# Kernel tuning notes

Measured on AMD Instinct MI355X. Metric: run time of the kernel, lower is better.

Reference implementation:

```python
import jax, jax.numpy as jnp
import numpy as np

E = 2048   # embed_dim
H = 16     # num query heads
D = E // H # head_dim = 128
B = 2
S = 2048


def setup_inputs() -> dict:
    key = jax.random.key(0)
    ks = jax.random.split(key, 12)
    sc = 0.02
    return {
        "input": jax.random.normal(ks[0], (B, S, E), jnp.float32),
        "kv": jax.random.normal(ks[1], (B, S, E), jnp.float32),
        "Wq": jax.random.normal(ks[2], (E, E), jnp.float32) * sc,
        "bq": jnp.zeros((E,), jnp.float32),
        "Wk": jax.random.normal(ks[3], (D, E), jnp.float32) * sc,
        "bk": jnp.zeros((D,), jnp.float32),
        "Wv": jax.random.normal(ks[4], (D, E), jnp.float32) * sc,
        "bv": jnp.zeros((D,), jnp.float32),
        "Wo": jax.random.normal(ks[5], (E, E), jnp.float32) * sc,
        "bo": jnp.zeros((E,), jnp.float32),
        "expanding_context": 0,
    }


def reference(input, kv, Wq, bq, Wk, bk, Wv, bv, Wo, bo, expanding_context):
    b, s, _ = input.shape
    # projections (torch Linear: x @ W.T + b)
    q = (input @ Wq.T + bq).reshape(b, s, H, D).transpose(0, 2, 1, 3)  # [B,H,S,D]
    k = kv @ Wk.T + bk  # [B,S,D] single KV head
    v = kv @ Wv.T + bv  # [B,S,D]
    # scores with single KV head broadcast across query heads
    scores = jnp.einsum('bhsd,btd->bhst', q, k) / jnp.sqrt(jnp.float32(D))
    causal = jnp.triu(jnp.ones((s, s), bool), k=1)  # True above diagonal
    scores = jnp.where(causal[None, None], jnp.float32(-jnp.inf), scores)
    attn = jax.nn.softmax(scores, axis=-1)
    out = jnp.einsum('bhst,btd->bhsd', attn, v)  # [B,H,S,D]
    out = out.transpose(0, 2, 1, 3).reshape(b, s, E)
    return out @ Wo.T + bo
```

## Files before the change

### kernel.cpp

```cpp
#include <hip/hip_runtime.h>

#define B_  2
#define S_  2048
#define E_  2048
#define H_  16
#define D_  128
#define BS_ (B_*S_)

typedef __bf16 bf16_t;
typedef __bf16 bf16x8 __attribute__((ext_vector_type(8)));
typedef __bf16 bf16x4 __attribute__((ext_vector_type(4)));
typedef float  f32x4  __attribute__((ext_vector_type(4)));
typedef float  f32x16 __attribute__((ext_vector_type(16)));

#define QSCALE 0.1275174131003543f

__device__ __forceinline__ void gld16(const bf16_t* g, bf16_t* l) {
    __builtin_amdgcn_global_load_lds(
        (const __attribute__((address_space(1))) void*)g,
        (__attribute__((address_space(3))) void*)l,
        16, 0, 0);
}

__global__ void cvt_all(const float* __restrict__ s0, const float* __restrict__ s1,
                        const float* __restrict__ s2, const float* __restrict__ s3,
                        const float* __restrict__ s4, const float* __restrict__ s5,
                        bf16_t* d0, bf16_t* d1, bf16_t* d2,
                        bf16_t* d3, bf16_t* d4, bf16_t* d5)
{
    long i = ((long)blockIdx.x * blockDim.x + threadIdx.x) * 4;
    const float* s; bf16_t* d;
    if      (i <  8388608) { s = s0; d = d0; }
    else if (i < 16777216) { s = s1; d = d1; i -=  8388608; }
    else if (i < 20971520) { s = s2; d = d2; i -= 16777216; }
    else if (i < 21233664) { s = s3; d = d3; i -= 20971520; }
    else if (i < 21495808) { s = s4; d = d4; i -= 21233664; }
    else                   { s = s5; d = d5; i -= 21495808; }
    float4 v = *(const float4*)(s + i);
    bf16x4 o;
    o[0] = (bf16_t)v.x; o[1] = (bf16_t)v.y; o[2] = (bf16_t)v.z; o[3] = (bf16_t)v.w;
    *(bf16x4*)(d + i) = o;
}

template<int EP>
__device__ __forceinline__ void gemm_tile64(
    const bf16_t* __restrict__ A, const bf16_t* __restrict__ W,
    const float* __restrict__ biasA, const float* __restrict__ biasB,
    float* __restrict__ Cf, bf16_t* __restrict__ Cb,
    int N, int K, float scale, int m0, int w_n0, int c_n0,
    bf16_t* As, bf16_t* Bs)
{
    const int tid  = threadIdx.x;
    const int wave = tid >> 6, lane = tid & 63;
    const int wm = wave >> 1, wn = wave & 1;
    const int lrow = lane & 15, quad = lane >> 4;
    const int r8 = lane >> 3, c8 = (lane & 7) << 3;

    f32x4 acc[4][2] = {};

    for (int k0 = 0; k0 < K; k0 += 64) {
        __syncthreads();
#pragma unroll
        for (int j = 0; j < 4; ++j) {
            int base = (wave * 4 + j) * 8;
            gld16(A + (size_t)(m0 + base + r8) * K + k0 + c8, &As[base * 64]);
        }
#pragma unroll
        for (int j = 0; j < 2; ++j) {
            int base = (wave * 2 + j) * 8;
            gld16(W + (size_t)(w_n0 + base + r8) * K + k0 + c8, &Bs[base * 64]);
        }
        __syncthreads();
#pragma unroll
        for (int ks = 0; ks < 2; ++ks) {
            bf16x8 af[4], bfr[2];
#pragma unroll
            for (int mt = 0; mt < 4; ++mt)
                af[mt] = *(const bf16x8*)&As[(wm * 64 + mt * 16 + lrow) * 64 + ks * 32 + quad * 8];
#pragma unroll
            for (int nt = 0; nt < 2; ++nt)
                bfr[nt] = *(const bf16x8*)&Bs[(wn * 32 + nt * 16 + lrow) * 64 + ks * 32 + quad * 8];
#pragma unroll
            for (int mt = 0; mt < 4; ++mt)
#pragma unroll
                for (int nt = 0; nt < 2; ++nt)
                    acc[mt][nt] = __builtin_amdgcn_mfma_f32_16x16x32_bf16(
                        af[mt], bfr[nt], acc[mt][nt], 0, 0, 0);
        }
    }

#pragma unroll
    for (int mt = 0; mt < 4; ++mt) {
#pragma unroll
        for (int nt = 0; nt < 2; ++nt) {
            int nn = wn * 32 + nt * 16 + lrow;
            int col = c_n0 + nn;
            float bvv = (EP == 1 && biasB && col >= 128) ? biasB[col - 128]
                                                         : biasA[col];
#pragma unroll
            for (int r = 0; r < 4; ++r) {
                int row = m0 + wm * 64 + mt * 16 + quad * 4 + r;
                float v = (acc[mt][nt][r] + bvv) * scale;
                if (EP == 0) Cf[(size_t)row * N + col] = v;
                else         Cb[(size_t)row * N + col] = (bf16_t)v;
            }
        }
    }
}

__global__ __launch_bounds__(256) void gemm_qkv(
    const bf16_t* __restrict__ xb, const bf16_t* __restrict__ kvb,
    const bf16_t* __restrict__ Wq, const bf16_t* __restrict__ Wkv,
    const float* __restrict__ bq, const float* __restrict__ bk,
    const float* __restrict__ bv,
    bf16_t* __restrict__ Qb, bf16_t* __restrict__ KVb)
{
    __shared__ __align__(16) bf16_t As[128 * 64];
    __shared__ __align__(16) bf16_t Bs[64 * 64];
    const int m0 = blockIdx.y * 128;
    if (blockIdx.x < 32) {
        int n0 = blockIdx.x * 64;
        gemm_tile64<1>(xb, Wq, bq, nullptr, nullptr, Qb, E_, E_, QSCALE,
                       m0, n0, n0, As, Bs);
    } else {
        int n0 = (blockIdx.x - 32) * 64;
        gemm_tile64<1>(kvb, Wkv, bk, bv, nullptr, KVb, 256, E_, 1.0f,
                       m0, n0, n0, As, Bs);
    }
}

__global__ __launch_bounds__(256) void gemm_o(
    const bf16_t* __restrict__ A, const bf16_t* __restrict__ W,
    const float* __restrict__ bias, float* __restrict__ Cf)
{
    __shared__ __align__(16) bf16_t As[128 * 64];
    __shared__ __align__(16) bf16_t Bs[64 * 64];
    int n0 = blockIdx.x * 64;
    gemm_tile64<0>(A, W, bias, nullptr, Cf, nullptr, E_, E_, 1.0f,
                   blockIdx.y * 128, n0, n0, As, Bs);
}

__global__ __launch_bounds__(256, 2) void mqa_attn(
    const bf16_t* __restrict__ Q, const bf16_t* __restrict__ KV,
    bf16_t* __restrict__ O)
{
    __shared__ __align__(16) bf16_t Kt[64][136];
    __shared__ __align__(16) bf16_t Vt[128][72];
    __shared__ float rsl[4][32];

    const int bx = blockIdx.x, h = blockIdx.y, b = blockIdx.z;
    const int qb = b ? bx : (15 - bx);
    const int tid = threadIdx.x, wave = tid >> 6, lane = tid & 63;
    const int ln = lane & 31, hi = lane >> 5;
    const int q0w = qb * 128 + wave * 32;

    const bf16_t* kvp = KV + (size_t)(b * S_) * 256;

    bf16x8 qf[8];
    {
        const bf16_t* qp = Q + ((size_t)(b * S_ + q0w + ln)) * E_ + h * D_ + hi * 8;
#pragma unroll
        for (int st = 0; st < 8; ++st) qf[st] = *(const bf16x8*)(qp + st * 16);
    }

    f32x16 oacc[4] = {};
    float rs = 0.f;

    const int ntiles = 2 * qb + 2;
    bf16x8 kreg[4], vreg[4];

#pragma unroll
    for (int i = 0; i < 4; ++i) {
        int c = tid + 256 * i;
        kreg[i] = *(const bf16x8*)(kvp + (size_t)(c >> 4) * 256 + ((c & 15) << 3));
        vreg[i] = *(const bf16x8*)(kvp + (size_t)(c & 63) * 256 + 128 + ((c >> 6) << 3));
    }

    for (int kt = 0; kt < ntiles; ++kt) {
        const int k_base = kt * 64;
        __syncthreads();
#pragma unroll
        for (int i = 0; i < 4; ++i) {
            int c = tid + 256 * i;
            *(bf16x8*)&Kt[c >> 4][(c & 15) << 3] = kreg[i];
            int n = c & 63, d0 = (c >> 6) << 3;
#pragma unroll
            for (int j = 0; j < 8; ++j) Vt[d0 + j][n] = vreg[i][j];
        }
        __syncthreads();
        if (kt + 1 < ntiles) {
            const int nb = (kt + 1) * 64;
#pragma unroll
            for (int i = 0; i < 4; ++i) {
                int c = tid + 256 * i;
                kreg[i] = *(const bf16x8*)(kvp + (size_t)(nb + (c >> 4)) * 256 + ((c & 15) << 3));
                vreg[i] = *(const bf16x8*)(kvp + (size_t)(nb + (c & 63)) * 256 + 128 + ((c >> 6) << 3));
            }
        }

        if (k_base <= q0w + 31) {
            f32x16 sc[2] = {f32x16{}, f32x16{}};
#pragma unroll
            for (int st = 0; st < 8; ++st) {
                bf16x8 qv = qf[st];
#pragma unroll
                for (int ct = 0; ct < 2; ++ct) {
                    bf16x8 kf = *(const bf16x8*)&Kt[ct * 32 + ln][st * 16 + hi * 8];
                    sc[ct] = __builtin_amdgcn_mfma_f32_32x32x16_bf16(kf, qv, sc[ct], 0, 0, 0);
                }
            }
            const int qi = q0w + ln;
            const bool diag = (k_base + 63 > q0w);
#pragma unroll
            for (int ct = 0; ct < 2; ++ct) {
#pragma unroll
                for (int r = 0; r < 16; ++r) {
                    float s = sc[ct][r];
                    if (diag) {
                        int kj = k_base + ct * 32 + (r & 3) + 8 * (r >> 2) + 4 * hi;
                        if (kj > qi) s = -1e30f;
                    }
                    float p = exp2f(fminf(s, 110.f));
                    rs += p;
                    sc[ct][r] = p;
                }
            }
            bf16x8 af[4];
#pragma unroll
            for (int ks = 0; ks < 4; ++ks) {
                const int c = ks >> 1, b8 = (ks & 1) * 8;
                union { bf16_t h[2]; unsigned u; } pk0, pk1, pk2, pk3;
                pk0.h[0] = (bf16_t)sc[c][b8 + 0]; pk0.h[1] = (bf16_t)sc[c][b8 + 1];
                pk1.h[0] = (bf16_t)sc[c][b8 + 2]; pk1.h[1] = (bf16_t)sc[c][b8 + 3];
                pk2.h[0] = (bf16_t)sc[c][b8 + 4]; pk2.h[1] = (bf16_t)sc[c][b8 + 5];
                pk3.h[0] = (bf16_t)sc[c][b8 + 6]; pk3.h[1] = (bf16_t)sc[c][b8 + 7];
                const unsigned U0 = pk0.u, U1 = pk1.u, U2 = pk2.u, U3 = pk3.u;
                const unsigned V0 = __shfl_xor(U0, 32);
                const unsigned V1 = __shfl_xor(U1, 32);
                const unsigned V2 = __shfl_xor(U2, 32);
                const unsigned V3 = __shfl_xor(U3, 32);
                union { unsigned u[4]; bf16x8 v; } W;
                W.u[0] = hi ? V2 : U0;
                W.u[1] = hi ? V3 : U1;
                W.u[2] = hi ? U2 : V0;
                W.u[3] = hi ? U3 : V1;
                af[ks] = W.v;
            }
#pragma unroll
            for (int ks = 0; ks < 4; ++ks)
#pragma unroll
                for (int t = 0; t < 4; ++t) {
                    bf16x8 vf = *(const bf16x8*)&Vt[t * 32 + ln][ks * 16 + hi * 8];
                    oacc[t] = __builtin_amdgcn_mfma_f32_32x32x16_bf16(af[ks], vf, oacc[t], 0, 0, 0);
                }
        }
    }

    rs += __shfl_xor(rs, 32);
    __syncthreads();
    if (lane < 32) rsl[wave][ln] = 1.0f / rs;
    __syncthreads();
#pragma unroll
    for (int t = 0; t < 4; ++t)
#pragma unroll
        for (int r = 0; r < 16; ++r) {
            int ro = (r & 3) + 8 * (r >> 2) + 4 * hi;
            O[((size_t)(b * S_ + q0w + ro)) * E_ + h * D_ + t * 32 + ln] =
                (bf16_t)(oacc[t][r] * rsl[wave][ro]);
        }
}

extern "C" void kernel_launch(void* const* d_in, const int* in_sizes, int n_in,
                              void* d_out, int out_size, void* d_ws, size_t ws_size,
                              hipStream_t stream)
{
    const float* x   = (const float*)d_in[0];
    const float* kv  = (const float*)d_in[1];
    const float* Wq  = (const float*)d_in[2];
    const float* bq  = (const float*)d_in[3];
    const float* Wk  = (const float*)d_in[4];
    const float* bk  = (const float*)d_in[5];
    const float* Wv  = (const float*)d_in[6];
    const float* bv  = (const float*)d_in[7];
    const float* Wo  = (const float*)d_in[8];
    const float* bo  = (const float*)d_in[9];
    float* out = (float*)d_out;

    bf16_t* p    = (bf16_t*)d_ws;
    bf16_t* xb   = p;  p += (size_t)BS_ * E_;
    bf16_t* kvb  = p;  p += (size_t)BS_ * E_;
    bf16_t* Wqb  = p;  p += (size_t)E_ * E_;
    bf16_t* Wkvb = p;  p += (size_t)2 * D_ * E_;
    bf16_t* Wob  = p;  p += (size_t)E_ * E_;
    bf16_t* Qb   = p;  p += (size_t)BS_ * E_;
    bf16_t* KVb  = p;  p += (size_t)BS_ * 256;
    bf16_t* Ob   = p;  p += (size_t)BS_ * E_;

    cvt_all<<<dim3(25088), dim3(256), 0, stream>>>(
        x, kv, Wq, Wk, Wv, Wo,
        xb, kvb, Wqb, Wkvb, Wkvb + (size_t)D_ * E_, Wob);

    gemm_qkv<<<dim3(36, BS_ / 128), 256, 0, stream>>>(
        xb, kvb, Wqb, Wkvb, bq, bk, bv, Qb, KVb);

    mqa_attn<<<dim3(S_ / 128, H_, B_), 256, 0, stream>>>(Qb, KVb, Ob);

    gemm_o<<<dim3(E_ / 64, BS_ / 128), 256, 0, stream>>>(Ob, Wob, bo, out);
}
```

Before: 358.5 us.

## Split attention KV tiles across wave pairs with LDS merge and async K loads

The attention kernel goes from 4 to 8 waves per block. Each pair of waves shares one 32-row query slice and handles alternating 64-key halves of a 128-key chunk, and the partial outputs and row sums are combined through LDS at the end. K tiles are loaded straight into a swizzled LDS layout with global_load_lds, and V is transposed with paired 32-bit stores. MFMA sections are wrapped in s_setprio, and the exp2 clamp is removed. The aim is more parallelism per block and less cost per tile on the long causal rows, at the price of a larger LDS footprint and an extra reduction step.

```diff
diff --git a/kernel.cpp b/kernel.cpp
--- a/kernel.cpp
+++ b/kernel.cpp
@@ -140,19 +140,22 @@
                    blockIdx.y * 128, n0, n0, As, Bs);
 }
 
-__global__ __launch_bounds__(256, 2) void mqa_attn(
+__global__ __launch_bounds__(512, 4) void mqa_attn(
     const bf16_t* __restrict__ Q, const bf16_t* __restrict__ KV,
     bf16_t* __restrict__ O)
 {
-    __shared__ __align__(16) bf16_t Kt[64][136];
-    __shared__ __align__(16) bf16_t Vt[128][72];
-    __shared__ float rsl[4][32];
+    __shared__ __align__(16) unsigned char SMEM[68608];
+    bf16_t* Ks = (bf16_t*)SMEM;
+    bf16_t (*Vt)[136] = (bf16_t(*)[136])(SMEM + 32768);
+    float* rsl = (float*)(SMEM + 67584);
+    float* mrg = (float*)SMEM;
 
     const int bx = blockIdx.x, h = blockIdx.y, b = blockIdx.z;
     const int qb = b ? bx : (15 - bx);
     const int tid = threadIdx.x, wave = tid >> 6, lane = tid & 63;
+    const int wq = wave >> 1, wk = wave & 1;
     const int ln = lane & 31, hi = lane >> 5;
-    const int q0w = qb * 128 + wave * 32;
+    const int q0w = qb * 128 + wq * 32;
 
     const bf16_t* kvp = KV + (size_t)(b * S_) * 256;
 
@@ -166,49 +169,63 @@
     f32x16 oacc[4] = {};
     float rs = 0.f;
 
-    const int ntiles = 2 * qb + 2;
-    bf16x8 kreg[4], vreg[4];
-
-#pragma unroll
-    for (int i = 0; i < 4; ++i) {
-        int c = tid + 256 * i;
-        kreg[i] = *(const bf16x8*)(kvp + (size_t)(c >> 4) * 256 + ((c & 15) << 3));
-        vreg[i] = *(const bf16x8*)(kvp + (size_t)(c & 63) * 256 + 128 + ((c >> 6) << 3));
-    }
-
-    for (int kt = 0; kt < ntiles; ++kt) {
+    const int nper = qb + 1;
+
+    bf16x8 vA[2], vB[2];
+    auto loadV = [&](int k0) {
+#pragma unroll
+        for (int i = 0; i < 2; ++i) {
+            int c = tid + 512 * i;
+            int n = (c & 63) * 2, d0 = (c >> 6) << 3;
+            const bf16_t* src = kvp + (size_t)(k0 + n) * 256 + 128 + d0;
+            vA[i] = *(const bf16x8*)src;
+            vB[i] = *(const bf16x8*)(src + 256);
+        }
+    };
+    loadV(0);
+
+    for (int p = 0; p < nper; ++p) {
+        const int k0 = p * 128;
+        __syncthreads();
+#pragma unroll
+        for (int i = 0; i < 2; ++i) {
+            int c = tid + 512 * i;
+            int n = (c & 63) * 2, d0 = (c >> 6) << 3;
+#pragma unroll
+            for (int j = 0; j < 8; ++j) {
+                union { bf16_t h[2]; unsigned u; } w2;
+                w2.h[0] = vA[i][j]; w2.h[1] = vB[i][j];
+                *(unsigned*)&Vt[d0 + j][n] = w2.u;
+            }
+        }
+#pragma unroll
+        for (int j = 0; j < 4; ++j) {
+            int r = (wave * 4 + j) * 4 + (lane >> 4);
+            int cl = (lane & 15) ^ (r & 7);
+            gld16(kvp + (size_t)(k0 + r) * 256 + cl * 8, Ks + (wave * 4 + j) * 512);
+        }
+        asm volatile("s_waitcnt vmcnt(0)" ::: "memory");
+        __syncthreads();
+        if (p + 1 < nper) loadV(k0 + 128);
+
+        const int kt = 2 * p + wk;
         const int k_base = kt * 64;
-        __syncthreads();
-#pragma unroll
-        for (int i = 0; i < 4; ++i) {
-            int c = tid + 256 * i;
-            *(bf16x8*)&Kt[c >> 4][(c & 15) << 3] = kreg[i];
-            int n = c & 63, d0 = (c >> 6) << 3;
-#pragma unroll
-            for (int j = 0; j < 8; ++j) Vt[d0 + j][n] = vreg[i][j];
-        }
-        __syncthreads();
-        if (kt + 1 < ntiles) {
-            const int nb = (kt + 1) * 64;
-#pragma unroll
-            for (int i = 0; i < 4; ++i) {
-                int c = tid + 256 * i;
-                kreg[i] = *(const bf16x8*)(kvp + (size_t)(nb + (c >> 4)) * 256 + ((c & 15) << 3));
-                vreg[i] = *(const bf16x8*)(kvp + (size_t)(nb + (c & 63)) * 256 + 128 + ((c >> 6) << 3));
-            }
-        }
-
         if (k_base <= q0w + 31) {
+            const int x8 = ln & 7;
             f32x16 sc[2] = {f32x16{}, f32x16{}};
+            __builtin_amdgcn_s_setprio(1);
 #pragma unroll
             for (int st = 0; st < 8; ++st) {
                 bf16x8 qv = qf[st];
 #pragma unroll
                 for (int ct = 0; ct < 2; ++ct) {
-                    bf16x8 kf = *(const bf16x8*)&Kt[ct * 32 + ln][st * 16 + hi * 8];
-                    sc[ct] = __builtin_amdgcn_mfma_f32_32x32x16_bf16(kf, qv, sc[ct], 0, 0, 0);
+                    const bf16_t* kb = Ks + (wk * 64 + ct * 32 + ln) * 128
+                                          + ((((st << 1) | hi) ^ x8) << 3);
+                    sc[ct] = __builtin_amdgcn_mfma_f32_32x32x16_bf16(
+                        *(const bf16x8*)kb, qv, sc[ct], 0, 0, 0);
                 }
             }
+            __builtin_amdgcn_s_setprio(0);
             const int qi = q0w + ln;
             const bool diag = (k_base + 63 > q0w);
 #pragma unroll
@@ -220,9 +237,9 @@
                         int kj = k_base + ct * 32 + (r & 3) + 8 * (r >> 2) + 4 * hi;
                         if (kj > qi) s = -1e30f;
                     }
-                    float p = exp2f(fminf(s, 110.f));
-                    rs += p;
-                    sc[ct][r] = p;
+                    float pv = exp2f(s);
+                    rs += pv;
+                    sc[ct][r] = pv;
                 }
             }
             bf16x8 af[4];
@@ -246,28 +263,55 @@
                 W.u[3] = hi ? U3 : V1;
                 af[ks] = W.v;
             }
+            __builtin_amdgcn_s_setprio(1);
 #pragma unroll
             for (int ks = 0; ks < 4; ++ks)
 #pragma unroll
                 for (int t = 0; t < 4; ++t) {
-                    bf16x8 vf = *(const bf16x8*)&Vt[t * 32 + ln][ks * 16 + hi * 8];
+                    bf16x8 vf = *(const bf16x8*)&Vt[t * 32 + ln][wk * 64 + ks * 16 + hi * 8];
                     oacc[t] = __builtin_amdgcn_mfma_f32_32x32x16_bf16(af[ks], vf, oacc[t], 0, 0, 0);
                 }
-        }
-    }
-
+            __builtin_amdgcn_s_setprio(0);
+        }
+    }
+
+    __syncthreads();
     rs += __shfl_xor(rs, 32);
+    if (lane < 32) rsl[wave * 32 + ln] = rs;
+    if (wk) {
+#pragma unroll
+        for (int t = 0; t < 4; ++t) {
+            union { f32x16 v; f32x4 q[4]; } u; u.v = oacc[t];
+            float* d = mrg + (size_t)(((wq << 2) + t) * 64 + lane) * 16;
+#pragma unroll
+            for (int r4 = 0; r4 < 4; ++r4) *(f32x4*)(d + r4 * 4) = u.q[r4];
+        }
+    }
     __syncthreads();
-    if (lane < 32) rsl[wave][ln] = 1.0f / rs;
-    __syncthreads();
-#pragma unroll
-    for (int t = 0; t < 4; ++t)
+    if (!wk) {
+        float inv[16];
 #pragma unroll
         for (int r = 0; r < 16; ++r) {
             int ro = (r & 3) + 8 * (r >> 2) + 4 * hi;
-            O[((size_t)(b * S_ + q0w + ro)) * E_ + h * D_ + t * 32 + ln] =
-                (bf16_t)(oacc[t][r] * rsl[wave][ro]);
-        }
+            inv[r] = 1.0f / (rsl[(wq * 2) * 32 + ro] + rsl[(wq * 2 + 1) * 32 + ro]);
+        }
+#pragma unroll
+        for (int t = 0; t < 4; ++t) {
+            union { f32x16 v; f32x4 q[4]; } u; u.v = oacc[t];
+            const float* d = mrg + (size_t)(((wq << 2) + t) * 64 + lane) * 16;
+#pragma unroll
+            for (int r4 = 0; r4 < 4; ++r4) {
+                f32x4 m = *(const f32x4*)(d + r4 * 4);
+                u.q[r4] += m;
+            }
+#pragma unroll
+            for (int r = 0; r < 16; ++r) {
+                int ro = (r & 3) + 8 * (r >> 2) + 4 * hi;
+                O[((size_t)(b * S_ + q0w + ro)) * E_ + h * D_ + t * 32 + ln] =
+                    (bf16_t)(u.v[r] * inv[r]);
+            }
+        }
+    }
 }
 
 extern "C" void kernel_launch(void* const* d_in, const int* in_sizes, int n_in,
@@ -303,7 +347,7 @@
     gemm_qkv<<<dim3(36, BS_ / 128), 256, 0, stream>>>(
         xb, kvb, Wqb, Wkvb, bq, bk, bv, Qb, KVb);
 
-    mqa_attn<<<dim3(S_ / 128, H_, B_), 256, 0, stream>>>(Qb, KVb, Ob);
+    mqa_attn<<<dim3(S_ / 128, H_, B_), 512, 0, stream>>>(Qb, KVb, Ob);
 
     gemm_o<<<dim3(E_ / 64, BS_ / 128), 256, 0, stream>>>(Ob, Wob, bo, out);
 }
```

New measurement: 457.2 us. 27.5% more time.

## Double-buffer K/V in LDS and overlap previous tile's PV with current QK

Applied to the files above, without the earlier changes.

The attention kernel now keeps two LDS buffers for K and V. It software-pipelines the loop so that the P·V MFMAs for the previous tile run before the barrier, while the next tile is staged and the tile after that is prefetched. MFMA sections are wrapped in s_setprio. The causal mask is split into separate diagonal and non-diagonal exp paths, and the row sum uses four partial accumulators to shorten the dependency chain. This doubles LDS use (about 72KB per block), which may pressure occupancy at two blocks per CU, and the extra carried state adds register pressure.

```diff
diff --git a/kernel.cpp b/kernel.cpp
--- a/kernel.cpp
+++ b/kernel.cpp
@@ -144,8 +144,8 @@
     const bf16_t* __restrict__ Q, const bf16_t* __restrict__ KV,
     bf16_t* __restrict__ O)
 {
-    __shared__ __align__(16) bf16_t Kt[64][136];
-    __shared__ __align__(16) bf16_t Vt[128][72];
+    __shared__ __align__(16) bf16_t Kt[2][64][136];
+    __shared__ __align__(16) bf16_t Vt[2][128][72];
     __shared__ float rsl[4][32];
 
     const int bx = blockIdx.x, h = blockIdx.y, b = blockIdx.z;
@@ -164,68 +164,97 @@
     }
 
     f32x16 oacc[4] = {};
-    float rs = 0.f;
-
-    const int ntiles = 2 * qb + 2;
+    bf16x8 af[4] = {};
+    float rs0 = 0.f, rs1 = 0.f, rs2 = 0.f, rs3 = 0.f;
+
+    const int NT = 2 * qb + 2;
+    const int Tw = (q0w + 31) >> 6;
+
     bf16x8 kreg[4], vreg[4];
-
-#pragma unroll
-    for (int i = 0; i < 4; ++i) {
-        int c = tid + 256 * i;
-        kreg[i] = *(const bf16x8*)(kvp + (size_t)(c >> 4) * 256 + ((c & 15) << 3));
-        vreg[i] = *(const bf16x8*)(kvp + (size_t)(c & 63) * 256 + 128 + ((c >> 6) << 3));
-    }
-
-    for (int kt = 0; kt < ntiles; ++kt) {
-        const int k_base = kt * 64;
-        __syncthreads();
+    auto loadKV = [&](int kt) {
+        const int k0 = kt * 64;
 #pragma unroll
         for (int i = 0; i < 4; ++i) {
             int c = tid + 256 * i;
-            *(bf16x8*)&Kt[c >> 4][(c & 15) << 3] = kreg[i];
+            kreg[i] = *(const bf16x8*)(kvp + (size_t)(k0 + (c >> 4)) * 256 + ((c & 15) << 3));
             int n = c & 63, d0 = (c >> 6) << 3;
-#pragma unroll
-            for (int j = 0; j < 8; ++j) Vt[d0 + j][n] = vreg[i][j];
-        }
+            vreg[i] = *(const bf16x8*)(kvp + (size_t)(k0 + n) * 256 + 128 + d0);
+        }
+    };
+    auto stageWrite = [&](int bb) {
+#pragma unroll
+        for (int i = 0; i < 4; ++i) {
+            int c = tid + 256 * i;
+            *(bf16x8*)&Kt[bb][c >> 4][(c & 15) << 3] = kreg[i];
+            int n = c & 63, d0 = (c >> 6) << 3;
+#pragma unroll
+            for (int j = 0; j < 8; ++j) Vt[bb][d0 + j][n] = vreg[i][j];
+        }
+    };
+    auto doPV = [&](int vb) {
+        __builtin_amdgcn_s_setprio(1);
+#pragma unroll
+        for (int ks = 0; ks < 4; ++ks)
+#pragma unroll
+            for (int dt = 0; dt < 4; ++dt) {
+                bf16x8 vf = *(const bf16x8*)&Vt[vb][dt * 32 + ln][ks * 16 + hi * 8];
+                oacc[dt] = __builtin_amdgcn_mfma_f32_32x32x16_bf16(af[ks], vf, oacc[dt], 0, 0, 0);
+            }
+        __builtin_amdgcn_s_setprio(0);
+    };
+
+    loadKV(0);
+    stageWrite(0);
+    if (NT > 1) loadKV(1);
+
+    for (int t = 0; t < NT; ++t) {
+        const int cur = t & 1;
+        if (t >= 1 && t - 1 <= Tw) doPV(cur ^ 1);
         __syncthreads();
-        if (kt + 1 < ntiles) {
-            const int nb = (kt + 1) * 64;
-#pragma unroll
-            for (int i = 0; i < 4; ++i) {
-                int c = tid + 256 * i;
-                kreg[i] = *(const bf16x8*)(kvp + (size_t)(nb + (c >> 4)) * 256 + ((c & 15) << 3));
-                vreg[i] = *(const bf16x8*)(kvp + (size_t)(nb + (c & 63)) * 256 + 128 + ((c >> 6) << 3));
-            }
-        }
-
-        if (k_base <= q0w + 31) {
+        if (t + 1 < NT) stageWrite(cur ^ 1);
+        if (t + 2 < NT) loadKV(t + 2);
+        if (t <= Tw) {
             f32x16 sc[2] = {f32x16{}, f32x16{}};
+            __builtin_amdgcn_s_setprio(1);
 #pragma unroll
             for (int st = 0; st < 8; ++st) {
                 bf16x8 qv = qf[st];
 #pragma unroll
                 for (int ct = 0; ct < 2; ++ct) {
-                    bf16x8 kf = *(const bf16x8*)&Kt[ct * 32 + ln][st * 16 + hi * 8];
+                    bf16x8 kf = *(const bf16x8*)&Kt[cur][ct * 32 + ln][st * 16 + hi * 8];
                     sc[ct] = __builtin_amdgcn_mfma_f32_32x32x16_bf16(kf, qv, sc[ct], 0, 0, 0);
                 }
             }
+            __builtin_amdgcn_s_setprio(0);
+            const int k_base = t * 64;
             const int qi = q0w + ln;
-            const bool diag = (k_base + 63 > q0w);
-#pragma unroll
-            for (int ct = 0; ct < 2; ++ct) {
-#pragma unroll
-                for (int r = 0; r < 16; ++r) {
-                    float s = sc[ct][r];
-                    if (diag) {
+            if (k_base + 63 > q0w) {
+#pragma unroll
+                for (int ct = 0; ct < 2; ++ct)
+#pragma unroll
+                    for (int r = 0; r < 16; ++r) {
                         int kj = k_base + ct * 32 + (r & 3) + 8 * (r >> 2) + 4 * hi;
-                        if (kj > qi) s = -1e30f;
+                        float s = (kj > qi) ? -1e30f : sc[ct][r];
+                        float pv = exp2f(fminf(s, 110.f));
+                        if ((r & 3) == 0) rs0 += pv;
+                        else if ((r & 3) == 1) rs1 += pv;
+                        else if ((r & 3) == 2) rs2 += pv;
+                        else rs3 += pv;
+                        sc[ct][r] = pv;
                     }
-                    float p = exp2f(fminf(s, 110.f));
-                    rs += p;
-                    sc[ct][r] = p;
-                }
-            }
-            bf16x8 af[4];
+            } else {
+#pragma unroll
+                for (int ct = 0; ct < 2; ++ct)
+#pragma unroll
+                    for (int r = 0; r < 16; ++r) {
+                        float pv = exp2f(fminf(sc[ct][r], 110.f));
+                        if ((r & 3) == 0) rs0 += pv;
+                        else if ((r & 3) == 1) rs1 += pv;
+                        else if ((r & 3) == 2) rs2 += pv;
+                        else rs3 += pv;
+                        sc[ct][r] = pv;
+                    }
+            }
 #pragma unroll
             for (int ks = 0; ks < 4; ++ks) {
                 const int c = ks >> 1, b8 = (ks & 1) * 8;
@@ -246,27 +275,22 @@
                 W.u[3] = hi ? U3 : V1;
                 af[ks] = W.v;
             }
-#pragma unroll
-            for (int ks = 0; ks < 4; ++ks)
-#pragma unroll
-                for (int t = 0; t < 4; ++t) {
-                    bf16x8 vf = *(const bf16x8*)&Vt[t * 32 + ln][ks * 16 + hi * 8];
-                    oacc[t] = __builtin_amdgcn_mfma_f32_32x32x16_bf16(af[ks], vf, oacc[t], 0, 0, 0);
-                }
-        }
-    }
-
+        }
+    }
+    if (Tw == NT - 1) doPV(1);
+
+    float rs = (rs0 + rs1) + (rs2 + rs3);
     rs += __shfl_xor(rs, 32);
     __syncthreads();
     if (lane < 32) rsl[wave][ln] = 1.0f / rs;
     __syncthreads();
 #pragma unroll
-    for (int t = 0; t < 4; ++t)
+    for (int dt = 0; dt < 4; ++dt)
 #pragma unroll
         for (int r = 0; r < 16; ++r) {
             int ro = (r & 3) + 8 * (r >> 2) + 4 * hi;
-            O[((size_t)(b * S_ + q0w + ro)) * E_ + h * D_ + t * 32 + ln] =
-                (bf16_t)(oacc[t][r] * rsl[wave][ro]);
+            O[((size_t)(b * S_ + q0w + ro)) * E_ + h * D_ + dt * 32 + ln] =
+                (bf16_t)(oacc[dt][r] * rsl[wave][ro]);
         }
 }
 
```

Result: no change. 356.6 us (-0.5%).
